# Kernel optimization log

Measured on AMD Instinct MI355X. Metric: run time of the kernel, lower is better.

The kernel has to match this reference:

```python
import jax, jax.numpy as jnp
import numpy as np

B, T, C, W, H, HID = 64, 1024, 256, 28, 28, 512


def setup_inputs() -> dict:
    key = jax.random.key(0)
    k1, k2, k3, k4, k5, k6 = jax.random.split(key, 6)
    text = jax.random.normal(k1, (B, T), dtype=jnp.float32)
    vision = jax.random.normal(k2, (B, C, W, H), dtype=jnp.float32)
    s1 = 1.0 / np.sqrt(T + C)
    s2 = 1.0 / np.sqrt(HID)
    W1 = jax.random.uniform(k3, (T + C, HID), jnp.float32, -s1, s1)
    b1 = jax.random.uniform(k4, (HID,), jnp.float32, -s1, s1)
    W2 = jax.random.uniform(k5, (HID, 1), jnp.float32, -s2, s2)
    b2 = jax.random.uniform(k6, (1,), jnp.float32, -s2, s2)
    return {"text": text, "vision": vision, "W1": W1, "b1": b1, "W2": W2, "b2": b2}


def reference(text, vision, W1, b1, W2, b2):
    b, c, w, h = vision.shape
    p = w * h
    # pixels in (i*height + j) order, matching the torch double loop / view
    pixels = vision.transpose(0, 2, 3, 1).reshape(b, p, c)  # (B, P, C)
    text_b = jnp.broadcast_to(text[:, None, :], (b, p, text.shape[1]))
    feat = jnp.concatenate([text_b, pixels], axis=-1)        # (B, P, T+C)
    hidden = jax.nn.relu(jnp.einsum("bpf,fh->bph", feat, W1) + b1)
    scores = (jnp.einsum("bph,ho->bpo", hidden, W2) + b2)[..., 0]  # (B, P)
    weights = jax.nn.softmax(scores, axis=1)                 # (B, P)
    pooled = jnp.einsum("bpc,bp->bc", pixels, weights)       # (B, C)
    return jnp.concatenate([pooled, text], axis=1)           # (B, C+T)
```

## Files before the change

kernel.cpp:

```cpp
#include <hip/hip_runtime.h>

#define BB  64
#define TT  1024
#define CC  256
#define PP  784
#define HID 512
#define FF  1280

typedef float v4f __attribute__((ext_vector_type(4)));
typedef short v8s __attribute__((ext_vector_type(8)));

__device__ inline unsigned int bf16_rne_bits(float x) {
    unsigned int u = __float_as_uint(x);
    unsigned int r = u + 0x7FFFu + ((u >> 16) & 1u);
    return r & 0xFFFF0000u;
}

__device__ inline void barrier_lds_only() {
    asm volatile("s_waitcnt lgkmcnt(0)" ::: "memory");
    __builtin_amdgcn_s_barrier();
}

__global__ __launch_bounds__(256) void k_w1t(const float* __restrict__ W1,
                                             unsigned short* __restrict__ w1t_hi,
                                             unsigned short* __restrict__ w1t_lo) {
    const int id = blockIdx.x * 256 + threadIdx.x;
    const int ks = id >> 11;
    const int h  = (id >> 2) & 511;
    const int g  = id & 3;
    const float* W1v = W1 + (size_t)TT * HID;
    unsigned int hw[4], lw[4];
    #pragma unroll
    for (int k = 0; k < 4; ++k) {
        const int c0 = ks * 32 + g * 8 + 2 * k;
        float x0 = W1v[(size_t)c0 * HID + h];
        float x1 = W1v[(size_t)(c0 + 1) * HID + h];
        unsigned int h0 = bf16_rne_bits(x0), h1 = bf16_rne_bits(x1);
        unsigned int l0 = bf16_rne_bits(x0 - __uint_as_float(h0));
        unsigned int l1 = bf16_rne_bits(x1 - __uint_as_float(h1));
        hw[k] = (h0 >> 16) | (h1 & 0xFFFF0000u);
        lw[k] = (l0 >> 16) | (l1 & 0xFFFF0000u);
    }
    *(int4*)(&w1t_hi[(size_t)id * 8]) = make_int4(hw[0], hw[1], hw[2], hw[3]);
    *(int4*)(&w1t_lo[(size_t)id * 8]) = make_int4(lw[0], lw[1], lw[2], lw[3]);
}

__global__ __launch_bounds__(512) void k_text_gemm(const float* __restrict__ text,
                                                   const float* __restrict__ W1,
                                                   float* __restrict__ tbp) {
    const int b  = blockIdx.x;
    const int ks = blockIdx.y;
    const int t  = threadIdx.x;
    __shared__ float st[128];
    if (t < 128) st[t] = text[b * TT + ks * 128 + t];
    __syncthreads();
    float acc = 0.f;
    const float* wp = W1 + (size_t)(ks * 128) * HID + t;
    #pragma unroll 4
    for (int k = 0; k < 128; ++k)
        acc = fmaf(st[k], wp[(size_t)k * HID], acc);
    tbp[(b * 8 + ks) * HID + t] = acc;
}

__global__ __launch_bounds__(256, 3) void k_vision_mfma(
        const float* __restrict__ vision,
        const unsigned short* __restrict__ w1t_hi,
        const unsigned short* __restrict__ w1t_lo,
        const float* __restrict__ b1,
        const float* __restrict__ W2,
        const float* __restrict__ tbp,
        float* __restrict__ spart) {
    const int ptile = blockIdx.x;
    const int hh    = blockIdx.y;
    const int b     = blockIdx.z;
    const int tid   = threadIdx.x;
    const int lane  = tid & 63;
    const int w     = tid >> 6;
    const int l15   = lane & 15, lg = lane >> 4;

    __shared__ char albuf[2][14336];
    __shared__ float sred[4 * 112];

    v4f acc[7][2];
    #pragma unroll
    for (int m = 0; m < 7; ++m) {
        acc[m][0] = (v4f){0.f, 0.f, 0.f, 0.f};
        acc[m][1] = (v4f){0.f, 0.f, 0.f, 0.f};
    }

    const size_t vbase = (size_t)b * (CC * PP) + ptile * 112;
    const int spx = tid >> 1, sch = tid & 1;
    const bool stg = (tid < 224);

    float xa[16], xb[16];

    #define A_LOAD(XV, KS) do { \
        _Pragma("unroll") for (int j = 0; j < 16; ++j) { \
            const int c_ = (KS) * 32 + sch * 16 + j; \
            XV[j] = vision[vbase + (size_t)c_ * PP + spx]; } } while (0)

    #define A_WRITE(BUF, XV) do { \
        unsigned int hw[8], lw[8]; \
        _Pragma("unroll") for (int q = 0; q < 8; ++q) { \
            unsigned int h0 = bf16_rne_bits(XV[2 * q]); \
            unsigned int h1 = bf16_rne_bits(XV[2 * q + 1]); \
            unsigned int l0 = bf16_rne_bits(XV[2 * q] - __uint_as_float(h0)); \
            unsigned int l1 = bf16_rne_bits(XV[2 * q + 1] - __uint_as_float(h1)); \
            hw[q] = (h0 >> 16) | (h1 & 0xFFFF0000u); \
            lw[q] = (l0 >> 16) | (l1 & 0xFFFF0000u); } \
        int4* ah = (int4*)(&albuf[BUF][0]) + (spx * 4 + sch * 2); \
        int4* al = (int4*)(&albuf[BUF][7168]) + (spx * 4 + sch * 2); \
        ah[0] = make_int4(hw[0], hw[1], hw[2], hw[3]); \
        ah[1] = make_int4(hw[4], hw[5], hw[6], hw[7]); \
        al[0] = make_int4(lw[0], lw[1], lw[2], lw[3]); \
        al[1] = make_int4(lw[4], lw[5], lw[6], lw[7]); } while (0)

    const int bfr = (hh * 128 + w * 32 + l15) * 32 + lg * 8;

    #define COMPUTE(KS, BUF) do { \
        const unsigned short* bph_ = w1t_hi + (size_t)(KS) * 16384 + bfr; \
        const unsigned short* bpl_ = w1t_lo + (size_t)(KS) * 16384 + bfr; \
        const v8s bh0 = *(const v8s*)(bph_); \
        const v8s bh1 = *(const v8s*)(bph_ + 512); \
        const v8s bl0 = *(const v8s*)(bpl_); \
        const v8s bl1 = *(const v8s*)(bpl_ + 512); \
        const char* ab_ = &albuf[BUF][0]; \
        v8s ahr[7]; \
        _Pragma("unroll") for (int m = 0; m < 7; ++m) \
            ahr[m] = *(const v8s*)(ab_ + (m * 16 + l15) * 64 + lg * 16); \
        _Pragma("unroll") for (int m = 0; m < 7; ++m) \
            acc[m][0] = __builtin_amdgcn_mfma_f32_16x16x32_bf16(ahr[m], bh0, acc[m][0], 0, 0, 0); \
        _Pragma("unroll") for (int m = 0; m < 7; ++m) \
            acc[m][1] = __builtin_amdgcn_mfma_f32_16x16x32_bf16(ahr[m], bh1, acc[m][1], 0, 0, 0); \
        _Pragma("unroll") for (int m = 0; m < 7; ++m) \
            acc[m][0] = __builtin_amdgcn_mfma_f32_16x16x32_bf16(ahr[m], bl0, acc[m][0], 0, 0, 0); \
        _Pragma("unroll") for (int m = 0; m < 7; ++m) \
            acc[m][1] = __builtin_amdgcn_mfma_f32_16x16x32_bf16(ahr[m], bl1, acc[m][1], 0, 0, 0); \
        _Pragma("unroll") for (int m = 0; m < 7; ++m) { \
            const v8s alr = *(const v8s*)(ab_ + 7168 + (m * 16 + l15) * 64 + lg * 16); \
            acc[m][0] = __builtin_amdgcn_mfma_f32_16x16x32_bf16(alr, bh0, acc[m][0], 0, 0, 0); \
            acc[m][1] = __builtin_amdgcn_mfma_f32_16x16x32_bf16(alr, bh1, acc[m][1], 0, 0, 0); \
        } } while (0)

    if (stg) { A_LOAD(xa, 0); A_LOAD(xb, 1); A_WRITE(0, xa); }
    barrier_lds_only();

    for (int s = 0; s < 8; s += 2) {
        if (stg && s + 2 < 8) A_LOAD(xa, s + 2);
        COMPUTE(s, 0);
        if (stg) A_WRITE(1, xb);
        barrier_lds_only();
        if (stg && s + 3 < 8) A_LOAD(xb, s + 3);
        COMPUTE(s + 1, 1);
        if (stg && s + 2 < 8) A_WRITE(0, xa);
        barrier_lds_only();
    }

    float tbn[2], w2n[2];
    #pragma unroll
    for (int nn = 0; nn < 2; ++nn) {
        const int h = hh * 128 + w * 32 + nn * 16 + l15;
        const float* tp = tbp + (size_t)b * 8 * HID + h;
        float tv = b1[h];
        #pragma unroll
        for (int q = 0; q < 8; ++q) tv += tp[q * HID];
        tbn[nn] = tv;
        w2n[nn] = W2[h];
    }
    #pragma unroll
    for (int m = 0; m < 7; ++m) {
        #pragma unroll
        for (int r = 0; r < 4; ++r) {
            float s = 0.f;
            #pragma unroll
            for (int nn = 0; nn < 2; ++nn)
                s += fmaxf(acc[m][nn][r] + tbn[nn], 0.f) * w2n[nn];
            s += __shfl_xor(s, 1, 64);
            s += __shfl_xor(s, 2, 64);
            s += __shfl_xor(s, 4, 64);
            s += __shfl_xor(s, 8, 64);
            if (l15 == 0) sred[w * 112 + m * 16 + lg * 4 + r] = s;
        }
    }
    __syncthreads();
    if (tid < 112) {
        float s = sred[tid] + sred[112 + tid] + sred[224 + tid] + sred[336 + tid];
        spart[((size_t)hh * BB + b) * PP + ptile * 112 + tid] = s;
    }
    #undef A_LOAD
    #undef A_WRITE
    #undef COMPUTE
}

__global__ __launch_bounds__(256) void k_softmax_copy(float* __restrict__ sw,
                                                      const float* __restrict__ text,
                                                      float* __restrict__ out) {
    const int b   = blockIdx.x;
    const int tid = threadIdx.x;
    const int lane = tid & 63, wid = tid >> 6;
    __shared__ float red[4];
    const size_t pl = (size_t)BB * PP;

    float v[4]; int cnt = 0;
    float m = -3.4e38f;
    for (int p = tid; p < PP; p += 256) {
        const size_t o = (size_t)b * PP + p;
        v[cnt] = sw[o] + sw[pl + o] + sw[2 * pl + o] + sw[3 * pl + o];
        m = fmaxf(m, v[cnt]); ++cnt;
    }
    #pragma unroll
    for (int off = 32; off > 0; off >>= 1) m = fmaxf(m, __shfl_xor(m, off, 64));
    if (lane == 0) red[wid] = m;
    __syncthreads();
    m = fmaxf(fmaxf(red[0], red[1]), fmaxf(red[2], red[3]));
    __syncthreads();

    float ssum = 0.f;
    for (int i = 0; i < cnt; ++i) { v[i] = expf(v[i] - m); ssum += v[i]; }
    #pragma unroll
    for (int off = 32; off > 0; off >>= 1) ssum += __shfl_xor(ssum, off, 64);
    if (lane == 0) red[wid] = ssum;
    __syncthreads();
    const float inv = 1.f / (red[0] + red[1] + red[2] + red[3]);

    cnt = 0;
    for (int p = tid; p < PP; p += 256) sw[(size_t)b * PP + p] = v[cnt++] * inv;

    for (int j = tid; j < TT; j += 256) out[b * FF + CC + j] = text[b * TT + j];
}

__global__ __launch_bounds__(256) void k_pool(const float* __restrict__ vision,
                                              const float* __restrict__ wts,
                                              float* __restrict__ out) {
    const int cg = blockIdx.x;
    const int b  = blockIdx.y;
    const int tid = threadIdx.x, lane = tid & 63, wid = tid >> 6;
    __shared__ float wl[PP];
    {
        const int i = tid * 4;
        if (i < PP) *(float4*)&wl[i] = *(const float4*)&wts[(size_t)b * PP + i];
    }
    __syncthreads();
    #pragma unroll
    for (int ci = 0; ci < 8; ++ci) {
        const int c = cg * 32 + wid * 8 + ci;
        const float* vr = vision + (size_t)b * (CC * PP) + (size_t)c * PP;
        float acc = 0.f;
        #pragma unroll
        for (int k = 0; k < 4; ++k) {
            const int p4 = (lane + 64 * k) * 4;
            if (p4 < PP) {
                const float4 vv = *(const float4*)(vr + p4);
                const float4 ww = *(const float4*)&wl[p4];
                acc = fmaf(vv.x, ww.x, acc);
                acc = fmaf(vv.y, ww.y, acc);
                acc = fmaf(vv.z, ww.z, acc);
                acc = fmaf(vv.w, ww.w, acc);
            }
        }
        #pragma unroll
        for (int off = 32; off > 0; off >>= 1) acc += __shfl_xor(acc, off, 64);
        if (lane == 0) out[b * FF + c] = acc;
    }
}

extern "C" void kernel_launch(void* const* d_in, const int* in_sizes, int n_in,
                              void* d_out, int out_size, void* d_ws, size_t ws_size,
                              hipStream_t stream) {
    const float* text   = (const float*)d_in[0];
    const float* vision = (const float*)d_in[1];
    const float* W1     = (const float*)d_in[2];
    const float* b1     = (const float*)d_in[3];
    const float* W2     = (const float*)d_in[4];
    float* out = (float*)d_out;

    float* tbp = (float*)d_ws;
    float* sw  = tbp + BB * 8 * HID;
    unsigned short* w1t_hi = (unsigned short*)(sw + 4 * BB * PP);
    unsigned short* w1t_lo = w1t_hi + 131072;

    k_w1t        <<<64, 256, 0, stream>>>(W1, w1t_hi, w1t_lo);
    k_text_gemm  <<<dim3(BB, 8), 512, 0, stream>>>(text, W1, tbp);
    k_vision_mfma<<<dim3(7, 4, BB), 256, 0, stream>>>(vision, w1t_hi, w1t_lo,
                                                      b1, W2, tbp, sw);
    k_softmax_copy<<<BB, 256, 0, stream>>>(sw, text, out);
    k_pool       <<<dim3(8, BB), 256, 0, stream>>>(vision, sw, out);
}
```

Before: 178.3 us.

## Widen vision MFMA blocks to 512 threads covering 256 hidden units with swizzled LDS

The vision GEMM block now uses 8 waves, so each block covers 256 hidden columns instead of 128. The grid's hidden-split dimension drops from 4 to 2, which halves redundant staging of the vision tile into LDS and halves the partial-score buffers that softmax must sum. The A-tile LDS layout gets an XOR swizzle to cut bank conflicts, and the MFMA issue order is interleaved per m-row so hi and lo fragments load just before use. In exchange, each block needs more registers and fewer blocks are launched, which may reduce occupancy and latency hiding.

Result: slower. 194.0 us (+8.8%).

```diff
diff --git a/kernel.cpp b/kernel.cpp
--- a/kernel.cpp
+++ b/kernel.cpp
@@ -62,7 +62,7 @@
     tbp[(b * 8 + ks) * HID + t] = acc;
 }
 
-__global__ __launch_bounds__(256, 3) void k_vision_mfma(
+__global__ __launch_bounds__(512, 2) void k_vision_mfma(
         const float* __restrict__ vision,
         const unsigned short* __restrict__ w1t_hi,
         const unsigned short* __restrict__ w1t_lo,
@@ -79,7 +79,7 @@
     const int l15   = lane & 15, lg = lane >> 4;
 
     __shared__ char albuf[2][14336];
-    __shared__ float sred[4 * 112];
+    __shared__ float sred[8 * 112];
 
     v4f acc[7][2];
     #pragma unroll
@@ -89,33 +89,32 @@
     }
 
     const size_t vbase = (size_t)b * (CC * PP) + ptile * 112;
-    const int spx = tid >> 1, sch = tid & 1;
-    const bool stg = (tid < 224);
-
-    float xa[16], xb[16];
+    const bool stg = (tid < 448);
+    const int spx = tid % 112;
+    const int scg = tid / 112;
+    const int swoff = (spx * 64 + scg * 16) ^ ((spx & 7) << 4);
+
+    float xa[8], xb[8];
 
     #define A_LOAD(XV, KS) do { \
-        _Pragma("unroll") for (int j = 0; j < 16; ++j) { \
-            const int c_ = (KS) * 32 + sch * 16 + j; \
+        _Pragma("unroll") for (int j = 0; j < 8; ++j) { \
+            const int c_ = (KS) * 32 + scg * 8 + j; \
             XV[j] = vision[vbase + (size_t)c_ * PP + spx]; } } while (0)
 
     #define A_WRITE(BUF, XV) do { \
-        unsigned int hw[8], lw[8]; \
-        _Pragma("unroll") for (int q = 0; q < 8; ++q) { \
+        unsigned int hw[4], lw[4]; \
+        _Pragma("unroll") for (int q = 0; q < 4; ++q) { \
             unsigned int h0 = bf16_rne_bits(XV[2 * q]); \
             unsigned int h1 = bf16_rne_bits(XV[2 * q + 1]); \
             unsigned int l0 = bf16_rne_bits(XV[2 * q] - __uint_as_float(h0)); \
             unsigned int l1 = bf16_rne_bits(XV[2 * q + 1] - __uint_as_float(h1)); \
             hw[q] = (h0 >> 16) | (h1 & 0xFFFF0000u); \
             lw[q] = (l0 >> 16) | (l1 & 0xFFFF0000u); } \
-        int4* ah = (int4*)(&albuf[BUF][0]) + (spx * 4 + sch * 2); \
-        int4* al = (int4*)(&albuf[BUF][7168]) + (spx * 4 + sch * 2); \
-        ah[0] = make_int4(hw[0], hw[1], hw[2], hw[3]); \
-        ah[1] = make_int4(hw[4], hw[5], hw[6], hw[7]); \
-        al[0] = make_int4(lw[0], lw[1], lw[2], lw[3]); \
-        al[1] = make_int4(lw[4], lw[5], lw[6], lw[7]); } while (0)
-
-    const int bfr = (hh * 128 + w * 32 + l15) * 32 + lg * 8;
+        *(int4*)(&albuf[BUF][swoff])        = make_int4(hw[0], hw[1], hw[2], hw[3]); \
+        *(int4*)(&albuf[BUF][7168 + swoff]) = make_int4(lw[0], lw[1], lw[2], lw[3]); } while (0)
+
+    const int bfr = (hh * 256 + w * 32 + l15) * 32 + lg * 8;
+    const int aswz = (l15 & 7) << 4;
 
     #define COMPUTE(KS, BUF) do { \
         const unsigned short* bph_ = w1t_hi + (size_t)(KS) * 16384 + bfr; \
@@ -125,21 +124,16 @@
         const v8s bl0 = *(const v8s*)(bpl_); \
         const v8s bl1 = *(const v8s*)(bpl_ + 512); \
         const char* ab_ = &albuf[BUF][0]; \
-        v8s ahr[7]; \
-        _Pragma("unroll") for (int m = 0; m < 7; ++m) \
-            ahr[m] = *(const v8s*)(ab_ + (m * 16 + l15) * 64 + lg * 16); \
-        _Pragma("unroll") for (int m = 0; m < 7; ++m) \
-            acc[m][0] = __builtin_amdgcn_mfma_f32_16x16x32_bf16(ahr[m], bh0, acc[m][0], 0, 0, 0); \
-        _Pragma("unroll") for (int m = 0; m < 7; ++m) \
-            acc[m][1] = __builtin_amdgcn_mfma_f32_16x16x32_bf16(ahr[m], bh1, acc[m][1], 0, 0, 0); \
-        _Pragma("unroll") for (int m = 0; m < 7; ++m) \
-            acc[m][0] = __builtin_amdgcn_mfma_f32_16x16x32_bf16(ahr[m], bl0, acc[m][0], 0, 0, 0); \
-        _Pragma("unroll") for (int m = 0; m < 7; ++m) \
-            acc[m][1] = __builtin_amdgcn_mfma_f32_16x16x32_bf16(ahr[m], bl1, acc[m][1], 0, 0, 0); \
         _Pragma("unroll") for (int m = 0; m < 7; ++m) { \
-            const v8s alr = *(const v8s*)(ab_ + 7168 + (m * 16 + l15) * 64 + lg * 16); \
-            acc[m][0] = __builtin_amdgcn_mfma_f32_16x16x32_bf16(alr, bh0, acc[m][0], 0, 0, 0); \
-            acc[m][1] = __builtin_amdgcn_mfma_f32_16x16x32_bf16(alr, bh1, acc[m][1], 0, 0, 0); \
+            const int ao_ = (((m * 16 + l15) * 64) + lg * 16) ^ aswz; \
+            const v8s ah = *(const v8s*)(ab_ + ao_); \
+            const v8s al = *(const v8s*)(ab_ + 7168 + ao_); \
+            acc[m][0] = __builtin_amdgcn_mfma_f32_16x16x32_bf16(ah, bh0, acc[m][0], 0, 0, 0); \
+            acc[m][1] = __builtin_amdgcn_mfma_f32_16x16x32_bf16(ah, bh1, acc[m][1], 0, 0, 0); \
+            acc[m][0] = __builtin_amdgcn_mfma_f32_16x16x32_bf16(ah, bl0, acc[m][0], 0, 0, 0); \
+            acc[m][1] = __builtin_amdgcn_mfma_f32_16x16x32_bf16(ah, bl1, acc[m][1], 0, 0, 0); \
+            acc[m][0] = __builtin_amdgcn_mfma_f32_16x16x32_bf16(al, bh0, acc[m][0], 0, 0, 0); \
+            acc[m][1] = __builtin_amdgcn_mfma_f32_16x16x32_bf16(al, bh1, acc[m][1], 0, 0, 0); \
         } } while (0)
 
     if (stg) { A_LOAD(xa, 0); A_LOAD(xb, 1); A_WRITE(0, xa); }
@@ -159,7 +153,7 @@
     float tbn[2], w2n[2];
     #pragma unroll
     for (int nn = 0; nn < 2; ++nn) {
-        const int h = hh * 128 + w * 32 + nn * 16 + l15;
+        const int h = hh * 256 + w * 32 + nn * 16 + l15;
         const float* tp = tbp + (size_t)b * 8 * HID + h;
         float tv = b1[h];
         #pragma unroll
@@ -184,7 +178,9 @@
     }
     __syncthreads();
     if (tid < 112) {
-        float s = sred[tid] + sred[112 + tid] + sred[224 + tid] + sred[336 + tid];
+        float s = 0.f;
+        #pragma unroll
+        for (int q = 0; q < 8; ++q) s += sred[q * 112 + tid];
         spart[((size_t)hh * BB + b) * PP + ptile * 112 + tid] = s;
     }
     #undef A_LOAD
@@ -205,7 +201,7 @@
     float m = -3.4e38f;
     for (int p = tid; p < PP; p += 256) {
         const size_t o = (size_t)b * PP + p;
-        v[cnt] = sw[o] + sw[pl + o] + sw[2 * pl + o] + sw[3 * pl + o];
+        v[cnt] = sw[o] + sw[pl + o];
         m = fmaxf(m, v[cnt]); ++cnt;
     }
     #pragma unroll
@@ -276,12 +272,12 @@
 
     float* tbp = (float*)d_ws;
     float* sw  = tbp + BB * 8 * HID;
-    unsigned short* w1t_hi = (unsigned short*)(sw + 4 * BB * PP);
+    unsigned short* w1t_hi = (unsigned short*)(sw + 2 * BB * PP);
     unsigned short* w1t_lo = w1t_hi + 131072;
 
     k_w1t        <<<64, 256, 0, stream>>>(W1, w1t_hi, w1t_lo);
     k_text_gemm  <<<dim3(BB, 8), 512, 0, stream>>>(text, W1, tbp);
-    k_vision_mfma<<<dim3(7, 4, BB), 256, 0, stream>>>(vision, w1t_hi, w1t_lo,
+    k_vision_mfma<<<dim3(7, 2, BB), 512, 0, stream>>>(vision, w1t_hi, w1t_lo,
                                                       b1, W2, tbp, sw);
     k_softmax_copy<<<BB, 256, 0, stream>>>(sw, text, out);
     k_pool       <<<dim3(8, BB), 256, 0, stream>>>(vision, sw, out);
```
